# Performance work log

Hardware: AMD Instinct MI355X
Metric: run time of the kernel (lower is better)

The kernel has to match this reference:

```python
import jax, jax.numpy as jnp
import numpy as np
import math

B, S, HID = 2, 2048, 4096
NH, NKV = 32, 8
HD = HID // NH  # 128
ROPE_BASE = 10000.0


def _rope_tables(seq_len, dim, base=ROPE_BASE):
    # ntk_alpha = 1 and mscale = 1 for seq_len <= training_seqlen
    inv_freq = 1.0 / (base ** (jnp.arange(0, dim, 2, dtype=jnp.float32) / dim))
    t = jnp.arange(seq_len, dtype=jnp.float32)
    freqs = jnp.einsum('i,j->ij', t, inv_freq)          # [S, dim/2]
    emb = jnp.concatenate([freqs, freqs], axis=-1)       # [S, dim]
    return jnp.cos(emb), jnp.sin(emb)


def setup_inputs() -> dict:
    key = jax.random.key(0)
    ks = jax.random.split(key, 5)
    hidden_states = jax.random.normal(ks[0], (B, S, HID), dtype=jnp.float32)
    # additive causal mask [B, 1, S, S]
    causal = jnp.where(jnp.tril(jnp.ones((S, S), dtype=bool)), 0.0, -1e9)
    attention_mask = jnp.broadcast_to(causal[None, None], (B, 1, S, S)).astype(jnp.float32)
    cos, sin = _rope_tables(S, HD)
    sc = 0.02
    Wq = jax.random.normal(ks[1], (HID, HID), dtype=jnp.float32) * sc
    Wkv = jax.random.normal(ks[2], (2 * NKV * HD, HID), dtype=jnp.float32) * sc
    Wd = jax.random.normal(ks[3], (HID, HID), dtype=jnp.float32) * sc
    bd = jnp.zeros((HID,), dtype=jnp.float32)
    return {"hidden_states": hidden_states, "attention_mask": attention_mask,
            "cos": cos, "sin": sin, "Wq": Wq, "Wkv": Wkv, "Wd": Wd, "bd": bd}


def _rotate_half(x):
    x1, x2 = jnp.split(x, 2, axis=-1)
    return jnp.concatenate([-x2, x1], axis=-1)


def reference(hidden_states, attention_mask, cos, sin, Wq, Wkv, Wd, bd):
    bsz, seq_len, _ = hidden_states.shape
    # Q projection: [B,S,HID] -> [B,NH,S,HD]
    q = (hidden_states @ Wq.T).reshape(bsz, seq_len, NH, HD).transpose(0, 2, 1, 3)
    # fused KV projection: [B,S,NKV,2*HD] -> split -> [B,NKV,S,HD] each
    kv = (hidden_states @ Wkv.T).reshape(bsz, seq_len, NKV, 2 * HD)
    k, v = jnp.split(kv, 2, axis=-1)
    k = k.transpose(0, 2, 1, 3)
    v = v.transpose(0, 2, 1, 3)
    # RoPE (broadcast cos/sin [S,HD] over batch and heads)
    c = cos[None, None, :, :]
    s = sin[None, None, :, :]
    q = q * c + _rotate_half(q) * s
    k = k * c + _rotate_half(k) * s
    # repeat_kv: expand KV heads to NH heads (group size NH//NKV)
    n_rep = NH // NKV
    k = jnp.repeat(k, n_rep, axis=1)  # [B,NH,S,HD]
    v = jnp.repeat(v, n_rep, axis=1)
    # attention
    scores = jnp.einsum('bhqd,bhkd->bhqk', q, k) / math.sqrt(HD)
    scores = scores + attention_mask[:, :, :, :seq_len]
    probs = jax.nn.softmax(scores.astype(jnp.float32), axis=-1).astype(q.dtype)
    attn = jnp.einsum('bhqk,bhkd->bhqd', probs, v)
    attn = attn.transpose(0, 2, 1, 3).reshape(bsz, seq_len, HID)
    return attn @ Wd.T + bd
```

## Files before the change

kernel.cpp:

```cpp
#include <hip/hip_runtime.h>

typedef __bf16 bf16;
typedef __bf16 bf16x4 __attribute__((ext_vector_type(4)));
typedef __bf16 bf16x8 __attribute__((ext_vector_type(8)));
typedef float floatx4 __attribute__((ext_vector_type(4)));

static constexpr int B_ = 2, S_ = 2048, HID_ = 4096, NH_ = 32, NKV_ = 8, HD_ = 128;

__device__ __forceinline__ void gll16(const void* g, void* l) {
    __builtin_amdgcn_global_load_lds(
        (const __attribute__((address_space(1))) void*)g,
        (__attribute__((address_space(3))) void*)l, 16, 0, 0);
}

__device__ __forceinline__ bf16x8 cvt8(const float* p) {
    float4 f0 = *(const float4*)p;
    float4 f1 = *(const float4*)(p + 4);
    bf16x8 v;
    v[0] = (bf16)f0.x; v[1] = (bf16)f0.y; v[2] = (bf16)f0.z; v[3] = (bf16)f0.w;
    v[4] = (bf16)f1.x; v[5] = (bf16)f1.y; v[6] = (bf16)f1.z; v[7] = (bf16)f1.w;
    return v;
}

__global__ __launch_bounds__(256) void cvt_kernel(const float* __restrict__ in,
                                                  bf16* __restrict__ out, int n8)
{
    int i = blockIdx.x * 256 + threadIdx.x;
    if (i >= n8) return;
    ((bf16x8*)out)[i] = cvt8(in + (size_t)i * 8);
}

template<int EPI>
__global__ __launch_bounds__(512, 2) void gemm256_kernel(
    const bf16* __restrict__ Ap, const bf16* __restrict__ Wp,
    const float* __restrict__ bias, void* __restrict__ Cp,
    bf16* __restrict__ Kw, bf16* __restrict__ Vtw,
    int M, int N, int K)
{
    __shared__ __attribute__((aligned(16))) bf16 As[4 * 8192];
    __shared__ __attribute__((aligned(16))) bf16 Bs[4 * 8192];

    const int tid = threadIdx.x;
    const int lane = tid & 63, wv = tid >> 6;
    const int lm = lane & 15, lq = lane >> 4;
    const int wr = (wv >> 2) * 128, wc = (wv & 3) * 64;
    const int m0 = blockIdx.y * 256, n0 = blockIdx.x * 256;

    const int NT = K >> 5;

    const int sr = lane >> 2;
    const int sch = (lane & 3) ^ ((lane >> 3) & 3);
    const bf16* aA0 = Ap + (size_t)(m0 + wv * 32 +      sr) * K + sch * 8;
    const bf16* aA1 = Ap + (size_t)(m0 + wv * 32 + 16 + sr) * K + sch * 8;
    const bf16* aB0 = Wp + (size_t)(n0 + wv * 32 +      sr) * K + sch * 8;
    const bf16* aB1 = Wp + (size_t)(n0 + wv * 32 + 16 + sr) * K + sch * 8;
    const int ub0 = wv * 1024;
    const int ub1 = wv * 1024 + 512;

    const int rko = (lq ^ ((lm >> 1) & 3)) * 8;

    floatx4 acc[8][4];
    #pragma unroll
    for (int i = 0; i < 8; i++)
        #pragma unroll
        for (int j = 0; j < 4; j++) acc[i][j] = (floatx4){0.f, 0.f, 0.f, 0.f};

    #pragma unroll
    for (int ts = 0; ts < 3; ++ts) {
        if (ts < NT) {
            const int sl = ts & 3;
            const size_t ko = (size_t)ts * 32;
            gll16(aA0 + ko, &As[sl * 8192 + ub0]);
            gll16(aA1 + ko, &As[sl * 8192 + ub1]);
            gll16(aB0 + ko, &Bs[sl * 8192 + ub0]);
            gll16(aB1 + ko, &Bs[sl * 8192 + ub1]);
        }
    }
    if (NT >= 3) asm volatile("s_waitcnt vmcnt(8)");
    else         asm volatile("s_waitcnt vmcnt(0)");
    __builtin_amdgcn_s_barrier();

    for (int t = 0; t < NT; ++t) {
        const bf16* Asl = As + (t & 3) * 8192;
        const bf16* Bsl = Bs + (t & 3) * 8192;
        const int ts = t + 3;
        const int sl = ts & 3;
        const bool st = ts < NT;
        const size_t ko = (size_t)ts * 32;

        bf16x8 af[4], bfr[4];
        #pragma unroll
        for (int i = 0; i < 4; i++)
            af[i] = *(const bf16x8*)&Asl[(wr + i * 16 + lm) * 32 + rko];
        #pragma unroll
        for (int j = 0; j < 4; j++)
            bfr[j] = *(const bf16x8*)&Bsl[(wc + j * 16 + lm) * 32 + rko];
        if (st) {
            gll16(aA0 + ko, &As[sl * 8192 + ub0]);
            gll16(aA1 + ko, &As[sl * 8192 + ub1]);
        }
        __builtin_amdgcn_s_barrier();
        asm volatile("s_waitcnt lgkmcnt(0)");
        __builtin_amdgcn_s_setprio(1);
        #pragma unroll
        for (int i = 0; i < 4; i++)
            #pragma unroll
            for (int j = 0; j < 4; j++)
                acc[i][j] = __builtin_amdgcn_mfma_f32_16x16x32_bf16(af[i], bfr[j], acc[i][j], 0, 0, 0);
        __builtin_amdgcn_s_setprio(0);
        __builtin_amdgcn_s_barrier();

        bf16x8 af2[4];
        #pragma unroll
        for (int i = 0; i < 4; i++)
            af2[i] = *(const bf16x8*)&Asl[(wr + 64 + i * 16 + lm) * 32 + rko];
        if (st) {
            gll16(aB0 + ko, &Bs[sl * 8192 + ub0]);
            gll16(aB1 + ko, &Bs[sl * 8192 + ub1]);
        }
        __builtin_amdgcn_s_barrier();
        asm volatile("s_waitcnt lgkmcnt(0)");
        __builtin_amdgcn_s_setprio(1);
        #pragma unroll
        for (int i = 0; i < 4; i++)
            #pragma unroll
            for (int j = 0; j < 4; j++)
                acc[4 + i][j] = __builtin_amdgcn_mfma_f32_16x16x32_bf16(af2[i], bfr[j], acc[4 + i][j], 0, 0, 0);
        __builtin_amdgcn_s_setprio(0);
        if (t < NT - 3)       asm volatile("s_waitcnt vmcnt(8)");
        else if (t == NT - 3) asm volatile("s_waitcnt vmcnt(4)");
        else                  asm volatile("s_waitcnt vmcnt(0)");
        __builtin_amdgcn_s_barrier();
    }

    #pragma unroll
    for (int i = 0; i < 8; i++)
        #pragma unroll
        for (int j = 0; j < 4; j++) {
            const int col = n0 + wc + j * 16 + lm;
            const int row0 = m0 + wr + i * 16 + lq * 4;
            if (EPI == 0) {
                #pragma unroll
                for (int r = 0; r < 4; r++)
                    ((bf16*)Cp)[(size_t)(row0 + r) * N + col] = (bf16)acc[i][j][r];
            } else if (EPI == 1) {
                const float bv = bias ? bias[col] : 0.f;
                #pragma unroll
                for (int r = 0; r < 4; r++)
                    ((float*)Cp)[(size_t)(row0 + r) * N + col] = acc[i][j][r] + bv;
            } else {
                const int head = col >> 8, off = col & 255;
                const int b = row0 >> 11, s0 = row0 & (S_ - 1);
                if (off < HD_) {
                    bf16* kp = Kw + ((size_t)(b * NKV_ + head) * S_ + s0) * HD_ + off;
                    #pragma unroll
                    for (int r = 0; r < 4; r++) kp[(size_t)r * HD_] = (bf16)acc[i][j][r];
                } else {
                    bf16x4 pv;
                    #pragma unroll
                    for (int r = 0; r < 4; r++) pv[r] = (bf16)acc[i][j][r];
                    *(bf16x4*)&Vtw[((size_t)(b * NKV_ + head) * HD_ + (off - HD_)) * S_ + s0] = pv;
                }
            }
        }
}

template<bool ABF, bool WBF, int EPI>
__global__ __launch_bounds__(256) void gemm_kernel(
    const void* __restrict__ Ap, const void* __restrict__ Wp,
    const float* __restrict__ bias, void* __restrict__ Cp,
    bf16* __restrict__ Kw, bf16* __restrict__ Vtw,
    int M, int N, int K)
{
    constexpr bool FAST = ABF && WBF;
    constexpr int STR = FAST ? 32 : 40;
    __shared__ __attribute__((aligned(16))) bf16 smem[2 * 128 * 40];
    bf16* Als = smem;
    bf16* Bls = smem + 128 * STR;

    const int tid = threadIdx.x;
    const int lane = tid & 63, wave = tid >> 6;
    const int lm = lane & 15, lq = lane >> 4;
    const int wr = (wave >> 1) * 64, wc = (wave & 1) * 64;
    const int m0 = blockIdx.y * 128, n0 = blockIdx.x * 128;

    floatx4 acc[4][4];
    #pragma unroll
    for (int i = 0; i < 4; i++)
        #pragma unroll
        for (int j = 0; j < 4; j++) acc[i][j] = (floatx4){0.f, 0.f, 0.f, 0.f};

    const int sr = tid >> 1;
    const int sc = (tid & 1) * 16;

    for (int k0 = 0; k0 < K; k0 += 32) {
        __syncthreads();
        if (FAST) {
            #pragma unroll
            for (int t = 0; t < 2; t++) {
                const int o = wave * 2048 + t * 1024 + lane * 16;
                const int row = o >> 6, ch = (o >> 4) & 3;
                const int ub = wave * 1024 + t * 512;
                gll16((const bf16*)Ap + (size_t)(m0 + row) * K + k0 + ch * 8, &Als[ub]);
                gll16((const bf16*)Wp + (size_t)(n0 + row) * K + k0 + ch * 8, &Bls[ub]);
            }
        } else {
            if (ABF) {
                const bf16* aptr = (const bf16*)Ap + (size_t)(m0 + sr) * K + sc + k0;
                *(bf16x8*)&Als[sr * STR + sc]     = *(const bf16x8*)(aptr);
                *(bf16x8*)&Als[sr * STR + sc + 8] = *(const bf16x8*)(aptr + 8);
            } else {
                const float* aptr = (const float*)Ap + (size_t)(m0 + sr) * K + sc + k0;
                *(bf16x8*)&Als[sr * STR + sc]     = cvt8(aptr);
                *(bf16x8*)&Als[sr * STR + sc + 8] = cvt8(aptr + 8);
            }
            const float* wptr = (const float*)Wp + (size_t)(n0 + sr) * K + sc + k0;
            *(bf16x8*)&Bls[sr * STR + sc]     = cvt8(wptr);
            *(bf16x8*)&Bls[sr * STR + sc + 8] = cvt8(wptr + 8);
        }
        __syncthreads();
        bf16x8 af[4], bfr[4];
        const int ko = lq * 8;
        #pragma unroll
        for (int i = 0; i < 4; i++) af[i]  = *(const bf16x8*)&Als[(wr + i * 16 + lm) * STR + ko];
        #pragma unroll
        for (int j = 0; j < 4; j++) bfr[j] = *(const bf16x8*)&Bls[(wc + j * 16 + lm) * STR + ko];
        #pragma unroll
        for (int i = 0; i < 4; i++)
            #pragma unroll
            for (int j = 0; j < 4; j++)
                acc[i][j] = __builtin_amdgcn_mfma_f32_16x16x32_bf16(af[i], bfr[j], acc[i][j], 0, 0, 0);
    }

    #pragma unroll
    for (int i = 0; i < 4; i++)
        #pragma unroll
        for (int j = 0; j < 4; j++) {
            const int col = n0 + wc + j * 16 + lm;
            const int row0 = m0 + wr + i * 16 + lq * 4;
            if (EPI == 0) {
                #pragma unroll
                for (int r = 0; r < 4; r++)
                    ((bf16*)Cp)[(size_t)(row0 + r) * N + col] = (bf16)acc[i][j][r];
            } else if (EPI == 1) {
                const float bv = bias ? bias[col] : 0.f;
                #pragma unroll
                for (int r = 0; r < 4; r++)
                    ((float*)Cp)[(size_t)(row0 + r) * N + col] = acc[i][j][r] + bv;
            } else {
                const int head = col >> 8, off = col & 255;
                const int b = row0 >> 11, s0 = row0 & (S_ - 1);
                if (off < HD_) {
                    bf16* kp = Kw + ((size_t)(b * NKV_ + head) * S_ + s0) * HD_ + off;
                    #pragma unroll
                    for (int r = 0; r < 4; r++) kp[(size_t)r * HD_] = (bf16)acc[i][j][r];
                } else {
                    bf16x4 pv;
                    #pragma unroll
                    for (int r = 0; r < 4; r++) pv[r] = (bf16)acc[i][j][r];
                    *(bf16x4*)&Vtw[((size_t)(b * NKV_ + head) * HD_ + (off - HD_)) * S_ + s0] = pv;
                }
            }
        }
}

__global__ __launch_bounds__(256) void rope_kernel(
    bf16* __restrict__ Qd, bf16* __restrict__ Kd,
    const float* __restrict__ cosd, const float* __restrict__ sind)
{
    const int idx = blockIdx.x * 256 + threadIdx.x;
    const int QROWS = B_ * S_ * NH_;
    const int d = idx & 63;
    const int row = idx >> 6;
    bf16* base; int s;
    if (row < QROWS) { base = Qd + (size_t)row * HD_; s = (row / NH_) & (S_ - 1); }
    else            { int rk = row - QROWS; base = Kd + (size_t)rk * HD_; s = rk & (S_ - 1); }
    const float c  = cosd[s * HD_ + d];
    const float sn = sind[s * HD_ + d];
    const float x1 = (float)base[d];
    const float x2 = (float)base[d + 64];
    base[d]      = (bf16)(x1 * c - x2 * sn);
    base[d + 64] = (bf16)(x2 * c + x1 * sn);
}

__global__ __launch_bounds__(512, 2) void attn_kernel(
    const bf16* __restrict__ Q, const bf16* __restrict__ Kw,
    const bf16* __restrict__ Vtw, bf16* __restrict__ O)
{
    const int bq = (int)gridDim.x - 1 - (int)blockIdx.x;
    const int h = blockIdx.y, b = blockIdx.z;
    const int kh = h >> 2;
    const int tid = threadIdx.x, wave = tid >> 6, lane = tid & 63;
    const int lm = lane & 15, lq = lane >> 4;

    __shared__ __attribute__((aligned(16))) bf16 Kls[64 * 128];
    __shared__ __attribute__((aligned(16))) bf16 Vls[128 * 64];
    __shared__ __attribute__((aligned(16))) bf16 Pls[8][16 * 72];

    const int q0 = bq * 128 + wave * 16;
    bf16x8 qa[4];
    {
        const bf16* qb = Q + ((size_t)(b * S_ + q0 + lm) * NH_ + h) * HD_;
        #pragma unroll
        for (int ks = 0; ks < 4; ks++) qa[ks] = *(const bf16x8*)(qb + ks * 32 + lq * 8);
    }

    float l_i[4];
    floatx4 oacc[8];
    #pragma unroll
    for (int r = 0; r < 4; r++) l_i[r] = 0.f;
    #pragma unroll
    for (int ct = 0; ct < 8; ct++) oacc[ct] = (floatx4){0.f, 0.f, 0.f, 0.f};

    const float C1 = 0.08838834764831845f * 1.4426950408889634f;
    const float C2 = -20.0f * 1.4426950408889634f;
    const bf16* Kbase = Kw  + (size_t)(b * NKV_ + kh) * S_ * HD_;
    const bf16* Vbase = Vtw + (size_t)(b * NKV_ + kh) * HD_ * S_;
    const int nkt = 2 * bq + 2;

    for (int it = 0; it < nkt; ++it) {
        const int kt = it * 64;
        __syncthreads();
        #pragma unroll
        for (int t = 0; t < 2; t++) {
            const int o = wave * 2048 + t * 1024 + lane * 16;
            const int ub = (wave * 2048 + t * 1024) / 2;
            { const int row = o >> 8, pos = (o >> 4) & 15, c = (pos - row) & 15;
              gll16(Kbase + (size_t)(kt + row) * HD_ + c * 8, &Kls[ub]); }
            { const int row = o >> 7, pos = (o >> 4) & 7, c = (pos - row) & 7;
              gll16(Vbase + (size_t)row * S_ + kt + c * 8, &Vls[ub]); }
        }
        __syncthreads();

        if (kt > q0 + 15) continue;
        const bool diag = (kt + 63 > q0);

        floatx4 sacc[4];
        #pragma unroll
        for (int nt = 0; nt < 4; nt++) sacc[nt] = (floatx4){0.f, 0.f, 0.f, 0.f};
        __builtin_amdgcn_s_setprio(1);
        #pragma unroll
        for (int nt = 0; nt < 4; nt++) {
            const int key = nt * 16 + lm;
            #pragma unroll
            for (int ks = 0; ks < 4; ks++) {
                bf16x8 kf = *(const bf16x8*)&Kls[key * 128 + ((ks * 4 + lq + key) & 15) * 8];
                sacc[nt] = __builtin_amdgcn_mfma_f32_16x16x32_bf16(qa[ks], kf, sacc[nt], 0, 0, 0);
            }
        }
        __builtin_amdgcn_s_setprio(0);

        if (diag) {
            #pragma unroll
            for (int r = 0; r < 4; r++) {
                const int qrow = q0 + lq * 4 + r;
                float lacc = 0.f;
                #pragma unroll
                for (int nt = 0; nt < 4; nt++) {
                    const int kcol = kt + nt * 16 + lm;
                    const float e = __builtin_amdgcn_exp2f(sacc[nt][r] * C1 + C2);
                    const float p = (kcol > qrow) ? 0.f : e;
                    lacc += p;
                    Pls[wave][(lq * 4 + r) * 72 + nt * 16 + lm] = (bf16)p;
                }
                l_i[r] += lacc;
            }
        } else {
            #pragma unroll
            for (int r = 0; r < 4; r++) {
                float lacc = 0.f;
                #pragma unroll
                for (int nt = 0; nt < 4; nt++) {
                    const float p = __builtin_amdgcn_exp2f(sacc[nt][r] * C1 + C2);
                    lacc += p;
                    Pls[wave][(lq * 4 + r) * 72 + nt * 16 + lm] = (bf16)p;
                }
                l_i[r] += lacc;
            }
        }

        __builtin_amdgcn_s_setprio(1);
        #pragma unroll
        for (int ks2 = 0; ks2 < 2; ks2++) {
            bf16x8 pa = *(const bf16x8*)&Pls[wave][lm * 72 + ks2 * 32 + lq * 8];
            #pragma unroll
            for (int ct = 0; ct < 8; ct++) {
                const int dr = ct * 16 + lm;
                bf16x8 vb = *(const bf16x8*)&Vls[dr * 64 + ((ks2 * 4 + lq + dr) & 7) * 8];
                oacc[ct] = __builtin_amdgcn_mfma_f32_16x16x32_bf16(pa, vb, oacc[ct], 0, 0, 0);
            }
        }
        __builtin_amdgcn_s_setprio(0);
    }

    #pragma unroll
    for (int r = 0; r < 4; r++) {
        float l = l_i[r];
        #pragma unroll
        for (int off = 1; off < 16; off <<= 1)
            l += __shfl_xor(l, off, 64);
        l_i[r] = l;
    }

    #pragma unroll
    for (int ct = 0; ct < 8; ct++)
        #pragma unroll
        for (int r = 0; r < 4; r++) {
            const int qrow = q0 + lq * 4 + r;
            O[(size_t)(b * S_ + qrow) * HID_ + h * HD_ + ct * 16 + lm]
                = (bf16)(oacc[ct][r] / l_i[r]);
        }
}

extern "C" void kernel_launch(void* const* d_in, const int* in_sizes, int n_in,
                              void* d_out, int out_size, void* d_ws, size_t ws_size,
                              hipStream_t stream)
{
    const float* hidden = (const float*)d_in[0];
    const float* cosd = (const float*)d_in[2];
    const float* sind = (const float*)d_in[3];
    const float* Wq   = (const float*)d_in[4];
    const float* Wkv  = (const float*)d_in[5];
    const float* Wd   = (const float*)d_in[6];
    const float* bd   = (const float*)d_in[7];
    float* out = (float*)d_out;

    const int M = B_ * S_;
    const int NKVC = 2 * NKV_ * HD_;
    bf16* Qw = (bf16*)d_out;
    bf16* wsb = (bf16*)d_ws;
    dim3 blk(256);
    dim3 blk512(512);

    const size_t E_HID  = (size_t)M * HID_;
    const size_t E_WKV  = (size_t)NKVC * HID_;
    const size_t E_K    = (size_t)B_ * NKV_ * S_ * HD_;
    const bool full = ws_size >= 2 * (3 * E_HID + E_WKV + 2 * E_K);

    const int rope_blocks = (B_ * S_ * NH_ + B_ * NKV_ * S_) * 64 / 256;

    if (full) {
        bf16* hb   = wsb;
        bf16* wqb  = hb   + E_HID;
        bf16* wkvb = wqb  + E_HID;
        bf16* wdb  = wkvb + E_WKV;
        bf16* Kw   = wdb  + E_HID;
        bf16* Vtw  = Kw   + E_K;
        bf16* Aw   = hb;

        cvt_kernel<<<dim3(E_HID / 8 / 256), blk, 0, stream>>>(hidden, hb,  (int)(E_HID / 8));
        cvt_kernel<<<dim3(E_HID / 8 / 256), blk, 0, stream>>>(Wq,     wqb, (int)(E_HID / 8));
        cvt_kernel<<<dim3(E_WKV / 8 / 256), blk, 0, stream>>>(Wkv,    wkvb,(int)(E_WKV / 8));
        cvt_kernel<<<dim3(E_HID / 8 / 256), blk, 0, stream>>>(Wd,     wdb, (int)(E_HID / 8));

        gemm256_kernel<0><<<dim3(HID_ / 256, M / 256), blk512, 0, stream>>>(
            hb, wqb, nullptr, Qw, nullptr, nullptr, M, HID_, HID_);
        gemm256_kernel<2><<<dim3(NKVC / 256, M / 256), blk512, 0, stream>>>(
            hb, wkvb, nullptr, nullptr, Kw, Vtw, M, NKVC, HID_);
        rope_kernel<<<dim3(rope_blocks), blk, 0, stream>>>(Qw, Kw, cosd, sind);
        attn_kernel<<<dim3(S_ / 128, NH_, B_), blk512, 0, stream>>>(Qw, Kw, Vtw, Aw);
        gemm256_kernel<1><<<dim3(HID_ / 256, M / 256), blk512, 0, stream>>>(
            Aw, wdb, bd, out, nullptr, nullptr, M, HID_, HID_);
    } else {
        bf16* Kw  = wsb;
        bf16* Vtw = Kw  + E_K;
        bf16* Aw  = Vtw + E_K;

        gemm_kernel<false, false, 0><<<dim3(HID_ / 128, M / 128), blk, 0, stream>>>(
            hidden, Wq, nullptr, Qw, nullptr, nullptr, M, HID_, HID_);
        gemm_kernel<false, false, 2><<<dim3(NKVC / 128, M / 128), blk, 0, stream>>>(
            hidden, Wkv, nullptr, nullptr, Kw, Vtw, M, NKVC, HID_);
        rope_kernel<<<dim3(rope_blocks), blk, 0, stream>>>(Qw, Kw, cosd, sind);
        attn_kernel<<<dim3(S_ / 128, NH_, B_), blk512, 0, stream>>>(Qw, Kw, Vtw, Aw);
        gemm_kernel<true, false, 1><<<dim3(HID_ / 128, M / 128), blk, 0, stream>>>(
            Aw, Wd, bd, out, nullptr, nullptr, M, HID_, HID_);
    }
}
```

Before: 817.1 us.

## Switch attention kernel to 32x32x16 MFMA with 4 waves of 32 query rows

Reworks the attention kernel so each wave handles 32 query rows with 32x32x16 bf16 MFMA instead of 16 rows with 16x16x32, and shrinks the block from 8 to 4 waves. Each wave's fragments are reused across more rows, so fewer LDS reads of K and V are needed per FLOP, and each thread loads 4 chunks of the K/V tile instead of 2. In exchange it uses more accumulator registers per thread, has fewer waves per block to hide latency, and does extra causal work on the diagonal because masking is now done per 32 rows.

```diff
diff --git a/kernel.cpp b/kernel.cpp
--- a/kernel.cpp
+++ b/kernel.cpp
@@ -4,6 +4,7 @@
 typedef __bf16 bf16x4 __attribute__((ext_vector_type(4)));
 typedef __bf16 bf16x8 __attribute__((ext_vector_type(8)));
 typedef float floatx4 __attribute__((ext_vector_type(4)));
+typedef float floatx16 __attribute__((ext_vector_type(16)));
 
 static constexpr int B_ = 2, S_ = 2048, HID_ = 4096, NH_ = 32, NKV_ = 8, HD_ = 128;
 
@@ -283,7 +284,7 @@
     base[d + 64] = (bf16)(x2 * c + x1 * sn);
 }
 
-__global__ __launch_bounds__(512, 2) void attn_kernel(
+__global__ __launch_bounds__(256) void attn_kernel(
     const bf16* __restrict__ Q, const bf16* __restrict__ Kw,
     const bf16* __restrict__ Vtw, bf16* __restrict__ O)
 {
@@ -291,26 +292,28 @@
     const int h = blockIdx.y, b = blockIdx.z;
     const int kh = h >> 2;
     const int tid = threadIdx.x, wave = tid >> 6, lane = tid & 63;
-    const int lm = lane & 15, lq = lane >> 4;
+    const int l5 = lane & 31, hi = lane >> 5;
 
     __shared__ __attribute__((aligned(16))) bf16 Kls[64 * 128];
     __shared__ __attribute__((aligned(16))) bf16 Vls[128 * 64];
-    __shared__ __attribute__((aligned(16))) bf16 Pls[8][16 * 72];
-
-    const int q0 = bq * 128 + wave * 16;
-    bf16x8 qa[4];
+    __shared__ __attribute__((aligned(16))) bf16 Pls[4][32 * 72];
+
+    const int q0 = bq * 128 + wave * 32;
+    bf16x8 qa[8];
     {
-        const bf16* qb = Q + ((size_t)(b * S_ + q0 + lm) * NH_ + h) * HD_;
-        #pragma unroll
-        for (int ks = 0; ks < 4; ks++) qa[ks] = *(const bf16x8*)(qb + ks * 32 + lq * 8);
-    }
-
-    float l_i[4];
-    floatx4 oacc[8];
-    #pragma unroll
-    for (int r = 0; r < 4; r++) l_i[r] = 0.f;
-    #pragma unroll
-    for (int ct = 0; ct < 8; ct++) oacc[ct] = (floatx4){0.f, 0.f, 0.f, 0.f};
+        const bf16* qb = Q + ((size_t)(b * S_ + q0 + l5) * NH_ + h) * HD_;
+        #pragma unroll
+        for (int c = 0; c < 8; c++) qa[c] = *(const bf16x8*)(qb + c * 16 + hi * 8);
+    }
+
+    float l16[16];
+    floatx16 oacc[4];
+    #pragma unroll
+    for (int r = 0; r < 16; r++) l16[r] = 0.f;
+    #pragma unroll
+    for (int dt = 0; dt < 4; dt++)
+        #pragma unroll
+        for (int r = 0; r < 16; r++) oacc[dt][r] = 0.f;
 
     const float C1 = 0.08838834764831845f * 1.4426950408889634f;
     const float C2 = -20.0f * 1.4426950408889634f;
@@ -322,9 +325,9 @@
         const int kt = it * 64;
         __syncthreads();
         #pragma unroll
-        for (int t = 0; t < 2; t++) {
-            const int o = wave * 2048 + t * 1024 + lane * 16;
-            const int ub = (wave * 2048 + t * 1024) / 2;
+        for (int t = 0; t < 4; t++) {
+            const int o = wave * 4096 + t * 1024 + lane * 16;
+            const int ub = (wave * 4096 + t * 1024) / 2;
             { const int row = o >> 8, pos = (o >> 4) & 15, c = (pos - row) & 15;
               gll16(Kbase + (size_t)(kt + row) * HD_ + c * 8, &Kls[ub]); }
             { const int row = o >> 7, pos = (o >> 4) & 7, c = (pos - row) & 7;
@@ -332,83 +335,87 @@
         }
         __syncthreads();
 
-        if (kt > q0 + 15) continue;
+        if (kt > q0 + 31) continue;
         const bool diag = (kt + 63 > q0);
 
-        floatx4 sacc[4];
-        #pragma unroll
-        for (int nt = 0; nt < 4; nt++) sacc[nt] = (floatx4){0.f, 0.f, 0.f, 0.f};
+        floatx16 sacc[2];
+        #pragma unroll
+        for (int nt = 0; nt < 2; nt++)
+            #pragma unroll
+            for (int r = 0; r < 16; r++) sacc[nt][r] = 0.f;
         __builtin_amdgcn_s_setprio(1);
         #pragma unroll
-        for (int nt = 0; nt < 4; nt++) {
-            const int key = nt * 16 + lm;
-            #pragma unroll
-            for (int ks = 0; ks < 4; ks++) {
-                bf16x8 kf = *(const bf16x8*)&Kls[key * 128 + ((ks * 4 + lq + key) & 15) * 8];
-                sacc[nt] = __builtin_amdgcn_mfma_f32_16x16x32_bf16(qa[ks], kf, sacc[nt], 0, 0, 0);
+        for (int nt = 0; nt < 2; nt++) {
+            const int key = nt * 32 + l5;
+            #pragma unroll
+            for (int c = 0; c < 8; c++) {
+                const int slot = (c * 2 + hi + key) & 15;
+                bf16x8 kf = *(const bf16x8*)&Kls[key * 128 + slot * 8];
+                sacc[nt] = __builtin_amdgcn_mfma_f32_32x32x16_bf16(qa[c], kf, sacc[nt], 0, 0, 0);
             }
         }
         __builtin_amdgcn_s_setprio(0);
 
         if (diag) {
             #pragma unroll
-            for (int r = 0; r < 4; r++) {
-                const int qrow = q0 + lq * 4 + r;
-                float lacc = 0.f;
-                #pragma unroll
-                for (int nt = 0; nt < 4; nt++) {
-                    const int kcol = kt + nt * 16 + lm;
+            for (int nt = 0; nt < 2; nt++) {
+                const int kcol = kt + nt * 32 + l5;
+                #pragma unroll
+                for (int r = 0; r < 16; r++) {
+                    const int row = (r & 3) + 8 * (r >> 2) + 4 * hi;
                     const float e = __builtin_amdgcn_exp2f(sacc[nt][r] * C1 + C2);
-                    const float p = (kcol > qrow) ? 0.f : e;
-                    lacc += p;
-                    Pls[wave][(lq * 4 + r) * 72 + nt * 16 + lm] = (bf16)p;
+                    const float p = (kcol > q0 + row) ? 0.f : e;
+                    l16[r] += p;
+                    Pls[wave][row * 72 + nt * 32 + l5] = (bf16)p;
                 }
-                l_i[r] += lacc;
             }
         } else {
             #pragma unroll
-            for (int r = 0; r < 4; r++) {
-                float lacc = 0.f;
-                #pragma unroll
-                for (int nt = 0; nt < 4; nt++) {
+            for (int nt = 0; nt < 2; nt++) {
+                #pragma unroll
+                for (int r = 0; r < 16; r++) {
+                    const int row = (r & 3) + 8 * (r >> 2) + 4 * hi;
                     const float p = __builtin_amdgcn_exp2f(sacc[nt][r] * C1 + C2);
-                    lacc += p;
-                    Pls[wave][(lq * 4 + r) * 72 + nt * 16 + lm] = (bf16)p;
+                    l16[r] += p;
+                    Pls[wave][row * 72 + nt * 32 + l5] = (bf16)p;
                 }
-                l_i[r] += lacc;
             }
         }
 
         __builtin_amdgcn_s_setprio(1);
-        #pragma unroll
-        for (int ks2 = 0; ks2 < 2; ks2++) {
-            bf16x8 pa = *(const bf16x8*)&Pls[wave][lm * 72 + ks2 * 32 + lq * 8];
-            #pragma unroll
-            for (int ct = 0; ct < 8; ct++) {
-                const int dr = ct * 16 + lm;
-                bf16x8 vb = *(const bf16x8*)&Vls[dr * 64 + ((ks2 * 4 + lq + dr) & 7) * 8];
-                oacc[ct] = __builtin_amdgcn_mfma_f32_16x16x32_bf16(pa, vb, oacc[ct], 0, 0, 0);
+        bf16x8 pa[4];
+        #pragma unroll
+        for (int c = 0; c < 4; c++)
+            pa[c] = *(const bf16x8*)&Pls[wave][l5 * 72 + c * 16 + hi * 8];
+        #pragma unroll
+        for (int dt = 0; dt < 4; dt++) {
+            const int dim = dt * 32 + l5;
+            #pragma unroll
+            for (int c = 0; c < 4; c++) {
+                const int slot = (c * 2 + hi + dim) & 7;
+                bf16x8 vb = *(const bf16x8*)&Vls[dim * 64 + slot * 8];
+                oacc[dt] = __builtin_amdgcn_mfma_f32_32x32x16_bf16(pa[c], vb, oacc[dt], 0, 0, 0);
             }
         }
         __builtin_amdgcn_s_setprio(0);
     }
 
     #pragma unroll
-    for (int r = 0; r < 4; r++) {
-        float l = l_i[r];
-        #pragma unroll
-        for (int off = 1; off < 16; off <<= 1)
+    for (int r = 0; r < 16; r++) {
+        float l = l16[r];
+        #pragma unroll
+        for (int off = 1; off < 32; off <<= 1)
             l += __shfl_xor(l, off, 64);
-        l_i[r] = l;
-    }
-
-    #pragma unroll
-    for (int ct = 0; ct < 8; ct++)
-        #pragma unroll
-        for (int r = 0; r < 4; r++) {
-            const int qrow = q0 + lq * 4 + r;
-            O[(size_t)(b * S_ + qrow) * HID_ + h * HD_ + ct * 16 + lm]
-                = (bf16)(oacc[ct][r] / l_i[r]);
+        l16[r] = l;
+    }
+
+    #pragma unroll
+    for (int dt = 0; dt < 4; dt++)
+        #pragma unroll
+        for (int r = 0; r < 16; r++) {
+            const int row = (r & 3) + 8 * (r >> 2) + 4 * hi;
+            O[(size_t)(b * S_ + q0 + row) * HID_ + h * HD_ + dt * 32 + l5]
+                = (bf16)(oacc[dt][r] / l16[r]);
         }
 }
 
@@ -458,7 +465,7 @@
         gemm256_kernel<2><<<dim3(NKVC / 256, M / 256), blk512, 0, stream>>>(
             hb, wkvb, nullptr, nullptr, Kw, Vtw, M, NKVC, HID_);
         rope_kernel<<<dim3(rope_blocks), blk, 0, stream>>>(Qw, Kw, cosd, sind);
-        attn_kernel<<<dim3(S_ / 128, NH_, B_), blk512, 0, stream>>>(Qw, Kw, Vtw, Aw);
+        attn_kernel<<<dim3(S_ / 128, NH_, B_), blk, 0, stream>>>(Qw, Kw, Vtw, Aw);
         gemm256_kernel<1><<<dim3(HID_ / 256, M / 256), blk512, 0, stream>>>(
             Aw, wdb, bd, out, nullptr, nullptr, M, HID_, HID_);
     } else {
@@ -471,7 +478,7 @@
         gemm_kernel<false, false, 2><<<dim3(NKVC / 128, M / 128), blk, 0, stream>>>(
             hidden, Wkv, nullptr, nullptr, Kw, Vtw, M, NKVC, HID_);
         rope_kernel<<<dim3(rope_blocks), blk, 0, stream>>>(Qw, Kw, cosd, sind);
-        attn_kernel<<<dim3(S_ / 128, NH_, B_), blk512, 0, stream>>>(Qw, Kw, Vtw, Aw);
+        attn_kernel<<<dim3(S_ / 128, NH_, B_), blk, 0, stream>>>(Qw, Kw, Vtw, Aw);
         gemm_kernel<true, false, 1><<<dim3(HID_ / 128, M / 128), blk, 0, stream>>>(
             Aw, Wd, bd, out, nullptr, nullptr, M, HID_, HID_);
     }
```

Result: slower. 906.5 us (+10.9%).
